# Performance work log

Measured on AMD Instinct MI355X. Metric: run time of the kernel, lower is better.

Reference implementation:

```python
import math
from itertools import combinations_with_replacement
import jax, jax.numpy as jnp
import numpy as np

# ---- static config (matches init_kwargs) ----
SPECIES_LIST = [1, 6, 8]
S = len(SPECIES_LIST)
N_MAX = 8
L_MAX = 4
CUTOFF = 5.0
B, N = 4, 512

SPECIES = jnp.asarray(SPECIES_LIST, dtype=jnp.int64 if jax.config.jax_enable_x64 else jnp.int32)
PAIR_IDS = np.array(list(combinations_with_replacement(range(S), 2)), dtype=np.int32)  # (P,2)
P = PAIR_IDS.shape[0]

# orthonormalization matrix W (deterministic buffer)
def _ortho_W(n_max):
    a = np.arange(1, n_max + 1, dtype=np.float64)
    Smat = np.sqrt((5 + 2 * a[:, None]) * (5 + 2 * a[None, :])) / (5 + a[:, None] + a[None, :])
    w, v = np.linalg.eigh(Smat)
    return (v @ np.diag(w ** -0.5) @ v.T).astype(np.float32)
W_ORTHO = jnp.asarray(_ortho_W(N_MAX))

# per-l power-spectrum prefactor pi*sqrt(8/(2l+1))
PS_NORM = jnp.asarray([math.pi * math.sqrt(8.0 / (2 * l + 1)) for l in range(L_MAX + 1)], dtype=jnp.float32)
# selector: which of the 25 flattened (l,m) components belong to degree l
_l_of_m = np.concatenate([np.full(2 * l + 1, l) for l in range(L_MAX + 1)])
L_SEL = jnp.asarray((_l_of_m[None, :] == np.arange(L_MAX + 1)[:, None]).astype(np.float32))  # (L,25)
# sqrt(2) on strict-upper (n,p) entries (applied before triu gather)
_offd = np.ones((N_MAX, N_MAX), dtype=np.float32)
_offd[np.triu_indices(N_MAX, 1)] = math.sqrt(2.0)
OFFD = jnp.asarray(_offd)
IU_R, IU_C = np.triu_indices(N_MAX)
PAIR_F = jnp.asarray(np.where(PAIR_IDS[:, 0] != PAIR_IDS[:, 1], math.sqrt(2.0), 1.0).astype(np.float32))


def real_sph_harm(u):
    """Real spherical harmonics (integral normalization, homogeneous polynomial form)
    for l=0..4, evaluated on u (..., 3). Returns (..., 25). Zero vector -> l>0 vanish."""
    x, y, z = u[..., 0], u[..., 1], u[..., 2]
    x2, y2, z2 = x * x, y * y, z * z
    r2 = x2 + y2 + z2
    pi = math.pi
    s = math.sqrt
    Y = [
        jnp.full_like(x, 0.5 * s(1 / pi)),
        s(3 / (4 * pi)) * y, s(3 / (4 * pi)) * z, s(3 / (4 * pi)) * x,
        0.5 * s(15 / pi) * x * y,
        0.5 * s(15 / pi) * y * z,
        0.25 * s(5 / pi) * (3 * z2 - r2),
        0.5 * s(15 / pi) * x * z,
        0.25 * s(15 / pi) * (x2 - y2),
        0.25 * s(35 / (2 * pi)) * y * (3 * x2 - y2),
        0.5 * s(105 / pi) * x * y * z,
        0.25 * s(21 / (2 * pi)) * y * (5 * z2 - r2),
        0.25 * s(7 / pi) * z * (5 * z2 - 3 * r2),
        0.25 * s(21 / (2 * pi)) * x * (5 * z2 - r2),
        0.25 * s(105 / pi) * z * (x2 - y2),
        0.25 * s(35 / (2 * pi)) * x * (x2 - 3 * y2),
        0.75 * s(35 / pi) * x * y * (x2 - y2),
        0.75 * s(35 / (2 * pi)) * y * z * (3 * x2 - y2),
        0.75 * s(5 / pi) * x * y * (7 * z2 - r2),
        0.75 * s(5 / (2 * pi)) * y * z * (7 * z2 - 3 * r2),
        (3.0 / 16.0) * s(1 / pi) * (35 * z2 * z2 - 30 * z2 * r2 + 3 * r2 * r2),
        0.75 * s(5 / (2 * pi)) * x * z * (7 * z2 - 3 * r2),
        (3.0 / 8.0) * s(5 / pi) * (x2 - y2) * (7 * z2 - r2),
        0.75 * s(35 / (2 * pi)) * x * z * (x2 - 3 * y2),
        (3.0 / 16.0) * s(35 / pi) * (x2 * x2 - 6 * x2 * y2 + y2 * y2),
    ]
    return jnp.stack(Y, axis=-1)


def soap_forward(pos, Z):
    b, n, _ = pos.shape
    # pairwise within each frame: dvec[b,i,j] = pos[b,i] - pos[b,j]  (dst - src)
    dvec = pos[:, :, None, :] - pos[:, None, :, :]          # (B,N,N,3)
    d2 = jnp.sum(dvec * dvec, axis=-1)
    dist = jnp.where(d2 > 0, jnp.sqrt(jnp.where(d2 > 0, d2, 1.0)), 0.0)
    u = dvec / jnp.where(dist > 0, dist, 1.0)[..., None]
    Y = real_sph_harm(u) * (4.0 * math.pi)                  # (B,N,N,25)
    # radial basis (l-independent in this module); cutoff mask folds in dist>=cutoff pairs
    alpha = jnp.arange(1, N_MAX + 1, dtype=pos.dtype)
    norm_factor = jnp.sqrt(CUTOFF ** (2 * alpha + 5) / (2 * alpha + 5))
    dr = jnp.maximum(CUTOFF - dist, 0.0)[..., None]
    basis = dr ** (alpha + 2) / norm_factor * (dist < CUTOFF).astype(pos.dtype)[..., None]
    g = basis @ W_ORTHO.T                                   # (B,N,N,n_max)
    # per-species scatter-add over source atoms j -> density coefficients c
    s_oh = (Z[..., None] == SPECIES).astype(pos.dtype)      # (B,N,S)
    c = jnp.einsum('bjs,bijn,bijm->bisnm', s_oh, g, Y)      # (B,N,S,n_max,25)
    # power spectrum: sum over m within each l
    ps = jnp.einsum('bisnm,bitpm,lm->bistlnp', c, c, L_SEL) # (B,N,S,S,L,n,n)
    ps = ps[:, :, PAIR_IDS[:, 0], PAIR_IDS[:, 1]]           # (B,N,P,L,n,n)
    ps = ps * PAIR_F[:, None, None, None] * PS_NORM[:, None, None] * OFFD
    desc = ps[..., IU_R, IU_C]                              # (B,N,P,L,36)
    return desc.reshape(b, n, -1)                           # (B,N,1080)


def setup_inputs() -> dict:
    key = jax.random.key(0)
    k1, k2 = jax.random.split(key)
    pos = jax.random.uniform(k1, (B, N, 3), dtype=jnp.float32) * 22.0
    Z = SPECIES[jax.random.randint(k2, (B, N), 0, S)]
    return {'pos': pos, 'Z': Z}


def reference(pos, Z):
    return soap_forward(pos, Z)
```

## Files before the change

kernel.cpp:

```cpp
#include <hip/hip_runtime.h>
#include <cmath>

#define NMAX   8
#define NM     25
#define ROWW   40
#define NOUT   1080
#define C2SZ   1440

struct Params {
    float W[NMAX * NMAX];
    float invnorm[NMAX];
    float ycoef[NM];
    float lscale[5];
    float pairf[6];
};

__device__ __forceinline__ void neighbor_compute(const Params& prm,
                                                 float dx, float dy, float dz,
                                                 float* __restrict__ row) {
    const float d2 = dx * dx + dy * dy + dz * dz;
    const float dist = sqrtf(d2);
    const float inv  = dist > 0.f ? 1.f / dist : 0.f;
    const float x = dx * inv, y = dy * inv, z = dz * inv;
    const float x2 = x * x, y2 = y * y, z2 = z * z;
    const float r2 = x2 + y2 + z2;

    const float dr = 5.f - dist;
    float bas[NMAX];
    float drp = dr * dr * dr;
#pragma unroll
    for (int a = 0; a < NMAX; ++a) { bas[a] = drp * prm.invnorm[a]; drp *= dr; }
    float g[NMAX];
#pragma unroll
    for (int n = 0; n < NMAX; ++n) {
        float acc = 0.f;
#pragma unroll
        for (int a = 0; a < NMAX; ++a) acc += bas[a] * prm.W[n * NMAX + a];
        g[n] = acc;
    }

    float Yv[NM];
    Yv[0]  = prm.ycoef[0];
    Yv[1]  = prm.ycoef[1]  * y;
    Yv[2]  = prm.ycoef[2]  * z;
    Yv[3]  = prm.ycoef[3]  * x;
    Yv[4]  = prm.ycoef[4]  * x * y;
    Yv[5]  = prm.ycoef[5]  * y * z;
    Yv[6]  = prm.ycoef[6]  * (3.f * z2 - r2);
    Yv[7]  = prm.ycoef[7]  * x * z;
    Yv[8]  = prm.ycoef[8]  * (x2 - y2);
    Yv[9]  = prm.ycoef[9]  * y * (3.f * x2 - y2);
    Yv[10] = prm.ycoef[10] * x * y * z;
    Yv[11] = prm.ycoef[11] * y * (5.f * z2 - r2);
    Yv[12] = prm.ycoef[12] * z * (5.f * z2 - 3.f * r2);
    Yv[13] = prm.ycoef[13] * x * (5.f * z2 - r2);
    Yv[14] = prm.ycoef[14] * z * (x2 - y2);
    Yv[15] = prm.ycoef[15] * x * (x2 - 3.f * y2);
    Yv[16] = prm.ycoef[16] * x * y * (x2 - y2);
    Yv[17] = prm.ycoef[17] * y * z * (3.f * x2 - y2);
    Yv[18] = prm.ycoef[18] * x * y * (7.f * z2 - r2);
    Yv[19] = prm.ycoef[19] * y * z * (7.f * z2 - 3.f * r2);
    Yv[20] = prm.ycoef[20] * (35.f * z2 * z2 - 30.f * z2 * r2 + 3.f * r2 * r2);
    Yv[21] = prm.ycoef[21] * x * z * (7.f * z2 - 3.f * r2);
    Yv[22] = prm.ycoef[22] * (x2 - y2) * (7.f * z2 - r2);
    Yv[23] = prm.ycoef[23] * x * z * (x2 - 3.f * y2);
    Yv[24] = prm.ycoef[24] * (x2 * x2 - 6.f * x2 * y2 + y2 * y2);

    float4* q = (float4*)row;
    q[0] = make_float4(g[0], g[1], g[2], g[3]);
    q[1] = make_float4(g[4], g[5], g[6], g[7]);
    q[2] = make_float4(Yv[0], Yv[8],  Yv[16], Yv[24]);
    q[3] = make_float4(Yv[1], Yv[9],  Yv[17], 0.f);
    q[4] = make_float4(Yv[2], Yv[10], Yv[18], 0.f);
    q[5] = make_float4(Yv[3], Yv[11], Yv[19], 0.f);
    q[6] = make_float4(Yv[4], Yv[12], Yv[20], 0.f);
    q[7] = make_float4(Yv[5], Yv[13], Yv[21], 0.f);
    q[8] = make_float4(Yv[6], Yv[14], Yv[22], 0.f);
    q[9] = make_float4(Yv[7], Yv[15], Yv[23], 0.f);
}

__global__ __launch_bounds__(64)
void soap_kernel(const float* __restrict__ pos, const int* __restrict__ Z,
                 float* __restrict__ out, Params prm) {
    __shared__ __align__(16) float gys[64 * ROWW];
    __shared__ float4 dA[64];
    __shared__ float4 dB[64];
    __shared__ __align__(16) float c2[C2SZ];
    __shared__ int spl[64];

    const int lane = threadIdx.x;
    const int site = blockIdx.x;
    const int jbase = (site >> 9) << 9;

    const float xi = pos[site * 3 + 0];
    const float yi = pos[site * 3 + 1];
    const float zi = pos[site * 3 + 2];

    {
        float4* c4 = (float4*)c2;
        const float4 zz4 = make_float4(0.f, 0.f, 0.f, 0.f);
#pragma unroll
        for (int i = 0; i < 5; ++i) c4[i * 64 + lane] = zz4;
        if (lane < 40) c4[320 + lane] = zz4;
    }

    const unsigned long long ltm = (1ull << lane) - 1ull;
    int mtot = 0;
#pragma unroll
    for (int it = 0; it < 8; ++it) {
        const int ja = jbase + it * 64 + lane;
        const float dx = xi - pos[ja * 3 + 0];
        const float dy = yi - pos[ja * 3 + 1];
        const float dz = zi - pos[ja * 3 + 2];
        const float d2 = dx * dx + dy * dy + dz * dz;
        const bool pr = d2 < 25.0f;
        const unsigned long long mk = __ballot(pr);
        if (pr) {
            const int sl = mtot + __popcll(mk & ltm);
            if (sl < 64) dA[sl] = make_float4(dx, dy, dz, (float)ja);
        }
        mtot += __popcll(mk);
    }
    const int M = mtot;

    const int n_own = lane & 7;
    const int mrow  = lane >> 3;
    float a0[4] = {0.f,0.f,0.f,0.f};
    float a1[4] = {0.f,0.f,0.f,0.f};
    float a2[4] = {0.f,0.f,0.f,0.f};

    if (M <= 64) {
        float4 v = make_float4(0.f, 0.f, 0.f, 0.f);
        int sp = -1;
        if (lane < M) {
            v = dA[lane];
            const int zz = Z[(int)v.w];
            sp = (zz == 1) ? 0 : (zz == 6) ? 1 : 2;
        }
        const unsigned long long b0 = __ballot(sp == 0);
        const unsigned long long b1 = __ballot(sp == 1);
        const unsigned long long b2 = __ballot(sp == 2);
        const int R1 = __popcll(b0);
        const int R2 = R1 + __popcll(b1);
        int np = -1;
        if (sp == 0)      np = __popcll(b0 & ltm);
        else if (sp == 1) np = R1 + __popcll(b1 & ltm);
        else if (sp == 2) np = R2 + __popcll(b2 & ltm);
        if (np >= 0) dB[np] = v;

        if (lane < M) {
            const float4 u = dB[lane];
            neighbor_compute(prm, u.x, u.y, u.z, &gys[lane * ROWW]);
        }

        const float* yb = &gys[8 + 4 * mrow];
#pragma unroll 2
        for (int sl = 0; sl < R1; ++sl) {
            const float g = gys[sl * ROWW + n_own];
            const float4 y4 = *(const float4*)&yb[sl * ROWW];
            a0[0] += g * y4.x; a0[1] += g * y4.y; a0[2] += g * y4.z; a0[3] += g * y4.w;
        }
#pragma unroll 2
        for (int sl = R1; sl < R2; ++sl) {
            const float g = gys[sl * ROWW + n_own];
            const float4 y4 = *(const float4*)&yb[sl * ROWW];
            a1[0] += g * y4.x; a1[1] += g * y4.y; a1[2] += g * y4.z; a1[3] += g * y4.w;
        }
#pragma unroll 2
        for (int sl = R2; sl < M; ++sl) {
            const float g = gys[sl * ROWW + n_own];
            const float4 y4 = *(const float4*)&yb[sl * ROWW];
            a2[0] += g * y4.x; a2[1] += g * y4.y; a2[2] += g * y4.z; a2[3] += g * y4.w;
        }
    } else {
        for (int it = 0; it < 8; ++it) {
            const int ja = jbase + it * 64 + lane;
            const float dx = xi - pos[ja * 3 + 0];
            const float dy = yi - pos[ja * 3 + 1];
            const float dz = zi - pos[ja * 3 + 2];
            const float d2 = dx * dx + dy * dy + dz * dz;
            const bool pr = d2 < 25.0f;
            const unsigned long long mk = __ballot(pr);
            const int cnt = __popcll(mk);
            if (pr) {
                const int sl = __popcll(mk & ltm);
                dA[sl] = make_float4(dx, dy, dz, 0.f);
                const int zz = Z[ja];
                spl[sl] = (zz == 1) ? 0 : (zz == 6) ? 1 : 2;
            }
            if (lane < cnt) {
                const float4 u = dA[lane];
                neighbor_compute(prm, u.x, u.y, u.z, &gys[lane * ROWW]);
            }
            const float* yb = &gys[8 + 4 * mrow];
            for (int sl = 0; sl < cnt; ++sl) {
                const int ss = spl[sl];
                const float g = gys[sl * ROWW + n_own];
                const float4 y4 = *(const float4*)&yb[sl * ROWW];
                if (ss == 0) {
                    a0[0] += g * y4.x; a0[1] += g * y4.y; a0[2] += g * y4.z; a0[3] += g * y4.w;
                } else if (ss == 1) {
                    a1[0] += g * y4.x; a1[1] += g * y4.y; a1[2] += g * y4.z; a1[3] += g * y4.w;
                } else {
                    a2[0] += g * y4.x; a2[1] += g * y4.y; a2[2] += g * y4.z; a2[3] += g * y4.w;
                }
            }
        }
    }

#pragma unroll
    for (int k = 0; k < 4; ++k) {
        const int m = mrow + 8 * k;
        if (m < NM) {
            const int l  = (int)sqrtf((float)m);
            const int kk = m - l * l;
            const int idx = l * 288 + n_own * 12 + kk;
            c2[idx      ] = a0[k];
            c2[idx +  96] = a1[k];
            c2[idx + 192] = a2[k];
        }
    }

#pragma unroll
    for (int it = 0; it < 17; ++it) {
        const int o = it * 64 + lane;
        if (o < NOUT) {
            const int q   = o / 180;
            const int rem = o - q * 180;
            const int l   = rem / 36;
            const int t   = rem - l * 36;
            const int n = (int)((17.0f - sqrtf((float)(289 - 8 * t))) * 0.5f);
            const int p = t - ((n * (17 - n)) >> 1) + n;
            const int s1 = (q < 3) ? 0 : ((q < 5) ? 1 : 2);
            const int s2 = (q < 3) ? q : ((q < 5) ? (q - 2) : 2);
            const float4* ra = (const float4*)&c2[l * 288 + s1 * 96 + n * 12];
            const float4* rb = (const float4*)&c2[l * 288 + s2 * 96 + p * 12];
            const float4 A0 = ra[0], B0 = rb[0];
            const float4 A1 = ra[1], B1 = rb[1];
            const float4 A2 = ra[2], B2 = rb[2];
            float sum = A0.x * B0.x + A0.y * B0.y + A0.z * B0.z + A0.w * B0.w
                      + A1.x * B1.x + A1.y * B1.y + A1.z * B1.z + A1.w * B1.w
                      + A2.x * B2.x + A2.y * B2.y + A2.z * B2.z + A2.w * B2.w;
            float sc = prm.pairf[q] * prm.lscale[l];
            if (n != p) sc *= 1.41421356237309515f;
            out[site * NOUT + o] = sum * sc;
        }
    }
}

extern "C" void kernel_launch(void* const* d_in, const int* in_sizes, int n_in,
                              void* d_out, int out_size, void* d_ws, size_t ws_size,
                              hipStream_t stream) {
    const float* pos = (const float*)d_in[0];
    const int*   Z   = (const int*)d_in[1];
    float*       out = (float*)d_out;
    const int nsite  = in_sizes[1];

    Params prm;

    double A[8][8], V[8][8];
    for (int i = 0; i < 8; ++i)
        for (int j = 0; j < 8; ++j) {
            const double ai = i + 1.0, aj = j + 1.0;
            A[i][j] = sqrt((5.0 + 2.0 * ai) * (5.0 + 2.0 * aj)) / (5.0 + ai + aj);
            V[i][j] = (i == j) ? 1.0 : 0.0;
        }
    for (int sweep = 0; sweep < 30; ++sweep) {
        for (int p = 0; p < 8; ++p)
            for (int q = p + 1; q < 8; ++q) {
                const double apq = A[p][q];
                if (fabs(apq) < 1e-300) continue;
                const double phi = 0.5 * atan2(2.0 * apq, A[q][q] - A[p][p]);
                const double c = cos(phi), s = sin(phi);
                for (int k = 0; k < 8; ++k) {
                    const double akp = A[k][p], akq = A[k][q];
                    A[k][p] = c * akp - s * akq;
                    A[k][q] = s * akp + c * akq;
                }
                for (int k = 0; k < 8; ++k) {
                    const double apk = A[p][k], aqk = A[q][k];
                    A[p][k] = c * apk - s * aqk;
                    A[q][k] = s * apk + c * aqk;
                }
                for (int k = 0; k < 8; ++k) {
                    const double vkp = V[k][p], vkq = V[k][q];
                    V[k][p] = c * vkp - s * vkq;
                    V[k][q] = s * vkp + c * vkq;
                }
            }
    }
    for (int i = 0; i < 8; ++i)
        for (int j = 0; j < 8; ++j) {
            double acc = 0.0;
            for (int k = 0; k < 8; ++k) acc += V[i][k] * V[j][k] / sqrt(A[k][k]);
            prm.W[i * 8 + j] = (float)acc;
        }

    for (int a = 0; a < 8; ++a)
        prm.invnorm[a] = (float)(1.0 / sqrt(pow(5.0, 2.0 * a + 7.0) / (2.0 * a + 7.0)));

    const double pi = 3.14159265358979323846;
    const double fp = 4.0 * pi;
    double yc[NM];
    yc[0]  = 0.5 * sqrt(1.0 / pi);
    yc[1]  = yc[2] = yc[3] = sqrt(3.0 / (4.0 * pi));
    yc[4]  = yc[5] = yc[7] = 0.5 * sqrt(15.0 / pi);
    yc[6]  = 0.25 * sqrt(5.0 / pi);
    yc[8]  = 0.25 * sqrt(15.0 / pi);
    yc[9]  = yc[15] = 0.25 * sqrt(35.0 / (2.0 * pi));
    yc[10] = 0.5 * sqrt(105.0 / pi);
    yc[11] = yc[13] = 0.25 * sqrt(21.0 / (2.0 * pi));
    yc[12] = 0.25 * sqrt(7.0 / pi);
    yc[14] = 0.25 * sqrt(105.0 / pi);
    yc[16] = 0.75 * sqrt(35.0 / pi);
    yc[17] = yc[23] = 0.75 * sqrt(35.0 / (2.0 * pi));
    yc[18] = 0.75 * sqrt(5.0 / pi);
    yc[19] = yc[21] = 0.75 * sqrt(5.0 / (2.0 * pi));
    yc[20] = 3.0 / 16.0 * sqrt(1.0 / pi);
    yc[22] = 3.0 / 8.0 * sqrt(5.0 / pi);
    yc[24] = 3.0 / 16.0 * sqrt(35.0 / pi);
    for (int m = 0; m < NM; ++m) prm.ycoef[m] = (float)(yc[m] * fp);

    for (int l = 0; l <= 4; ++l) prm.lscale[l] = (float)(pi * sqrt(8.0 / (2.0 * l + 1.0)));
    const float rt2 = 1.41421356237309515f;
    prm.pairf[0] = 1.f; prm.pairf[1] = rt2; prm.pairf[2] = rt2;
    prm.pairf[3] = 1.f; prm.pairf[4] = rt2; prm.pairf[5] = 1.f;

    soap_kernel<<<nsite, 64, 0, stream>>>(pos, Z, out, prm);
}
```

Before: 16.84 us.

## Stage batch positions and species in shared memory; merge species accumulation loops

Each block now loads the whole 512-atom position and species slab for its batch into shared memory with vectorized float4/int4 loads. Neighbor search and species lookup then read LDS instead of scattered global loads, and the buffers are aliased to keep the LDS footprint unchanged. The three per-species accumulation loops become one loop that prefetches the next row and branches on the species range. This adds a redundant 8 KB global load per block and extra branch work in the inner loop. Launch bounds now also state one block per CU minimum.

```diff
diff --git a/kernel.cpp b/kernel.cpp
--- a/kernel.cpp
+++ b/kernel.cpp
@@ -79,45 +79,53 @@
     q[9] = make_float4(Yv[7], Yv[15], Yv[23], 0.f);
 }
 
-__global__ __launch_bounds__(64)
+__global__ __launch_bounds__(64, 1)
 void soap_kernel(const float* __restrict__ pos, const int* __restrict__ Z,
                  float* __restrict__ out, Params prm) {
-    __shared__ __align__(16) float gys[64 * ROWW];
+    __shared__ __align__(16) float shA[64 * ROWW];
+    __shared__ __align__(16) float shB[C2SZ];
     __shared__ float4 dA[64];
     __shared__ float4 dB[64];
-    __shared__ __align__(16) float c2[C2SZ];
     __shared__ int spl[64];
 
     const int lane = threadIdx.x;
     const int site = blockIdx.x;
     const int jbase = (site >> 9) << 9;
-
-    const float xi = pos[site * 3 + 0];
-    const float yi = pos[site * 3 + 1];
-    const float zi = pos[site * 3 + 2];
+    const unsigned long long ltm = (1ull << lane) - 1ull;
 
     {
-        float4* c4 = (float4*)c2;
-        const float4 zz4 = make_float4(0.f, 0.f, 0.f, 0.f);
-#pragma unroll
-        for (int i = 0; i < 5; ++i) c4[i * 64 + lane] = zz4;
-        if (lane < 40) c4[320 + lane] = zz4;
-    }
-
-    const unsigned long long ltm = (1ull << lane) - 1ull;
+        const float4* pg = (const float4*)(pos + jbase * 3);
+        const int4*   zg = (const int4*)(Z + jbase);
+        const float4 p0 = pg[lane],       p1 = pg[64 + lane],  p2 = pg[128 + lane];
+        const float4 p3 = pg[192 + lane], p4 = pg[256 + lane], p5 = pg[320 + lane];
+        const int4   z0 = zg[lane],       z1 = zg[64 + lane];
+        float4* pl = (float4*)shA;
+        int4*   zl = (int4*)shB;
+        pl[lane]       = p0; pl[64 + lane]  = p1; pl[128 + lane] = p2;
+        pl[192 + lane] = p3; pl[256 + lane] = p4; pl[320 + lane] = p5;
+        zl[lane] = z0; zl[64 + lane] = z1;
+    }
+    const float* pL = shA;
+    const int*   zL = (const int*)shB;
+
+    const int jsite = site & 511;
+    const float xi = pL[jsite * 3 + 0];
+    const float yi = pL[jsite * 3 + 1];
+    const float zi = pL[jsite * 3 + 2];
+
     int mtot = 0;
 #pragma unroll
     for (int it = 0; it < 8; ++it) {
-        const int ja = jbase + it * 64 + lane;
-        const float dx = xi - pos[ja * 3 + 0];
-        const float dy = yi - pos[ja * 3 + 1];
-        const float dz = zi - pos[ja * 3 + 2];
+        const int jl = it * 64 + lane;
+        const float dx = xi - pL[jl * 3 + 0];
+        const float dy = yi - pL[jl * 3 + 1];
+        const float dz = zi - pL[jl * 3 + 2];
         const float d2 = dx * dx + dy * dy + dz * dz;
         const bool pr = d2 < 25.0f;
         const unsigned long long mk = __ballot(pr);
         if (pr) {
             const int sl = mtot + __popcll(mk & ltm);
-            if (sl < 64) dA[sl] = make_float4(dx, dy, dz, (float)ja);
+            if (sl < 64) dA[sl] = make_float4(dx, dy, dz, (float)jl);
         }
         mtot += __popcll(mk);
     }
@@ -134,7 +142,7 @@
         int sp = -1;
         if (lane < M) {
             v = dA[lane];
-            const int zz = Z[(int)v.w];
+            const int zz = zL[(int)v.w];
             sp = (zz == 1) ? 0 : (zz == 6) ? 1 : 2;
         }
         const unsigned long long b0 = __ballot(sp == 0);
@@ -148,36 +156,57 @@
         else if (sp == 2) np = R2 + __popcll(b2 & ltm);
         if (np >= 0) dB[np] = v;
 
+        {
+            float4* c4 = (float4*)shB;
+            const float4 z4 = make_float4(0.f, 0.f, 0.f, 0.f);
+#pragma unroll
+            for (int i = 0; i < 6; ++i) {
+                const int j = i * 64 + lane;
+                if (j < 360) c4[j] = z4;
+            }
+        }
+
         if (lane < M) {
             const float4 u = dB[lane];
-            neighbor_compute(prm, u.x, u.y, u.z, &gys[lane * ROWW]);
-        }
-
-        const float* yb = &gys[8 + 4 * mrow];
-#pragma unroll 2
-        for (int sl = 0; sl < R1; ++sl) {
-            const float g = gys[sl * ROWW + n_own];
-            const float4 y4 = *(const float4*)&yb[sl * ROWW];
-            a0[0] += g * y4.x; a0[1] += g * y4.y; a0[2] += g * y4.z; a0[3] += g * y4.w;
-        }
-#pragma unroll 2
-        for (int sl = R1; sl < R2; ++sl) {
-            const float g = gys[sl * ROWW + n_own];
-            const float4 y4 = *(const float4*)&yb[sl * ROWW];
-            a1[0] += g * y4.x; a1[1] += g * y4.y; a1[2] += g * y4.z; a1[3] += g * y4.w;
-        }
-#pragma unroll 2
-        for (int sl = R2; sl < M; ++sl) {
-            const float g = gys[sl * ROWW + n_own];
-            const float4 y4 = *(const float4*)&yb[sl * ROWW];
-            a2[0] += g * y4.x; a2[1] += g * y4.y; a2[2] += g * y4.z; a2[3] += g * y4.w;
+            neighbor_compute(prm, u.x, u.y, u.z, &shA[lane * ROWW]);
+        }
+
+        const float* yb = &shA[8 + 4 * mrow];
+        float gq = 0.f;
+        float4 yq = make_float4(0.f, 0.f, 0.f, 0.f);
+        if (M > 0) { gq = shA[n_own]; yq = *(const float4*)&yb[0]; }
+        for (int sl = 0; sl < M; ++sl) {
+            float gn = 0.f;
+            float4 yn = make_float4(0.f, 0.f, 0.f, 0.f);
+            const int nx = sl + 1;
+            if (nx < M) { gn = shA[nx * ROWW + n_own]; yn = *(const float4*)&yb[nx * ROWW]; }
+            if (sl < R1) {
+                a0[0] += gq * yq.x; a0[1] += gq * yq.y; a0[2] += gq * yq.z; a0[3] += gq * yq.w;
+            } else if (sl < R2) {
+                a1[0] += gq * yq.x; a1[1] += gq * yq.y; a1[2] += gq * yq.z; a1[3] += gq * yq.w;
+            } else {
+                a2[0] += gq * yq.x; a2[1] += gq * yq.y; a2[2] += gq * yq.z; a2[3] += gq * yq.w;
+            }
+            gq = gn; yq = yn;
         }
     } else {
+        {
+            float4* c4 = (float4*)shB;
+            const float4 z4 = make_float4(0.f, 0.f, 0.f, 0.f);
+#pragma unroll
+            for (int i = 0; i < 6; ++i) {
+                const int j = i * 64 + lane;
+                if (j < 360) c4[j] = z4;
+            }
+        }
+        const float gxi = pos[site * 3 + 0];
+        const float gyi = pos[site * 3 + 1];
+        const float gzi = pos[site * 3 + 2];
         for (int it = 0; it < 8; ++it) {
             const int ja = jbase + it * 64 + lane;
-            const float dx = xi - pos[ja * 3 + 0];
-            const float dy = yi - pos[ja * 3 + 1];
-            const float dz = zi - pos[ja * 3 + 2];
+            const float dx = gxi - pos[ja * 3 + 0];
+            const float dy = gyi - pos[ja * 3 + 1];
+            const float dz = gzi - pos[ja * 3 + 2];
             const float d2 = dx * dx + dy * dy + dz * dz;
             const bool pr = d2 < 25.0f;
             const unsigned long long mk = __ballot(pr);
@@ -190,12 +219,12 @@
             }
             if (lane < cnt) {
                 const float4 u = dA[lane];
-                neighbor_compute(prm, u.x, u.y, u.z, &gys[lane * ROWW]);
-            }
-            const float* yb = &gys[8 + 4 * mrow];
+                neighbor_compute(prm, u.x, u.y, u.z, &shA[lane * ROWW]);
+            }
+            const float* yb = &shA[8 + 4 * mrow];
             for (int sl = 0; sl < cnt; ++sl) {
                 const int ss = spl[sl];
-                const float g = gys[sl * ROWW + n_own];
+                const float g = shA[sl * ROWW + n_own];
                 const float4 y4 = *(const float4*)&yb[sl * ROWW];
                 if (ss == 0) {
                     a0[0] += g * y4.x; a0[1] += g * y4.y; a0[2] += g * y4.z; a0[3] += g * y4.w;
@@ -215,9 +244,9 @@
             const int l  = (int)sqrtf((float)m);
             const int kk = m - l * l;
             const int idx = l * 288 + n_own * 12 + kk;
-            c2[idx      ] = a0[k];
-            c2[idx +  96] = a1[k];
-            c2[idx + 192] = a2[k];
+            shB[idx      ] = a0[k];
+            shB[idx +  96] = a1[k];
+            shB[idx + 192] = a2[k];
         }
     }
 
@@ -233,8 +262,8 @@
             const int p = t - ((n * (17 - n)) >> 1) + n;
             const int s1 = (q < 3) ? 0 : ((q < 5) ? 1 : 2);
             const int s2 = (q < 3) ? q : ((q < 5) ? (q - 2) : 2);
-            const float4* ra = (const float4*)&c2[l * 288 + s1 * 96 + n * 12];
-            const float4* rb = (const float4*)&c2[l * 288 + s2 * 96 + p * 12];
+            const float4* ra = (const float4*)&shB[l * 288 + s1 * 96 + n * 12];
+            const float4* rb = (const float4*)&shB[l * 288 + s2 * 96 + p * 12];
             const float4 A0 = ra[0], B0 = rb[0];
             const float4 A1 = ra[1], B1 = rb[1];
             const float4 A2 = ra[2], B2 = rb[2];
```

Measured after the change: 18.23 us. 1.08x slower.
